# Kernel tuning notes

Hardware: AMD Instinct MI355X
Metric: run time of the kernel (lower is better)

The kernel has to match this reference:

```python
import jax, jax.numpy as jnp
import numpy as np

HIDDEN = 512
HEADS = 8
HEAD_DIM = HIDDEN // HEADS
B, S = 4, 2048
EPS = 1e-5


def setup_inputs() -> dict:
    key = jax.random.key(0)
    ks = jax.random.split(key, 12)
    sc = 1.0 / np.sqrt(HIDDEN)
    return {
        "query": jax.random.normal(ks[0], (B, S, HIDDEN), jnp.float32),
        "key": jax.random.normal(ks[1], (B, S, HIDDEN), jnp.float32),
        "value": jax.random.normal(ks[2], (B, S, HIDDEN), jnp.float32),
        "mask": jnp.ones((B, S), jnp.int32),
        "Wq": jax.random.normal(ks[3], (HIDDEN, HIDDEN), jnp.float32) * sc,
        "bq": jnp.zeros((HIDDEN,), jnp.float32),
        "Wk": jax.random.normal(ks[4], (HIDDEN, HIDDEN), jnp.float32) * sc,
        "bk": jnp.zeros((HIDDEN,), jnp.float32),
        "Wv": jax.random.normal(ks[5], (HIDDEN, HIDDEN), jnp.float32) * sc,
        "bv": jnp.zeros((HIDDEN,), jnp.float32),
        "Wo": jax.random.normal(ks[6], (HIDDEN, HIDDEN), jnp.float32) * sc,
        "bo": jnp.zeros((HIDDEN,), jnp.float32),
        "temperature": jnp.ones((HEADS,), jnp.float32),
        "gamma": jnp.ones((HIDDEN,), jnp.float32),
        "beta": jnp.zeros((HIDDEN,), jnp.float32),
    }


def _split_heads(x):  # (B,S,H*D) -> (B,H,S,D)
    b, s, _ = x.shape
    return x.reshape(b, s, HEADS, HEAD_DIM).transpose(0, 2, 1, 3)


def _l1_scores(Q, K):
    # Manhattan distance dist[b,h,i,j] = sum_d |Q[b,h,i,d] - K[b,h,j,d]|
    # accumulated via scan over head_dim to avoid a (B,H,S,S,D) tensor.
    Qd = jnp.moveaxis(Q, -1, 0)  # (D,B,H,S)
    Kd = jnp.moveaxis(K, -1, 0)
    init = jnp.zeros(Q.shape[:3] + (K.shape[2],), Q.dtype)  # (B,H,S,S)

    def step(acc, qk):
        q, k = qk  # (B,H,S)
        return acc + jnp.abs(q[..., :, None] - k[..., None, :]), None

    dist, _ = jax.lax.scan(step, init, (Qd, Kd))
    return dist


def reference(query, key, value, mask, Wq, bq, Wk, bk, Wv, bv, Wo, bo,
              temperature, gamma, beta):
    Q = _split_heads(query @ Wq.T + bq)
    K = _split_heads(key @ Wk.T + bk)
    V = _split_heads(value @ Wv.T + bv)

    dist = _l1_scores(Q, K)                                 # (B,H,S,S)
    scores = -dist * temperature[None, :, None, None]
    m = mask[:, None, None, :]                              # (B,1,1,S)
    scores = jnp.where(m == 0, jnp.float32(-1e9), scores)
    attn = jax.nn.softmax(scores, axis=-1)                  # (B,H,S,S)

    out = jnp.einsum("bhij,bhjd->bhid", attn, V)            # (B,H,S,D)
    out = out.transpose(0, 2, 1, 3).reshape(query.shape)    # (B,S,HIDDEN)
    out = out @ Wo.T + bo

    res = out + query
    mu = jnp.mean(res, axis=-1, keepdims=True)
    var = jnp.var(res, axis=-1, keepdims=True)
    out = (res - mu) * jax.lax.rsqrt(var + EPS) * gamma + beta
    return out, attn
```

## Files before the change

### kernel.cpp

```cpp
#include <hip/hip_runtime.h>
#include <math.h>

#define BB 4
#define SS 2048
#define NH 8
#define HD 64
#define HID 512
#define EPSV 1e-5f

#define NROWS (BB * SS)
#define QKV_ELEMS (BB * NH * SS * HD)
#define TOTROWS (BB * NH * SS)
#define NJT 16

typedef __attribute__((ext_vector_type(8))) short short8;
typedef __attribute__((ext_vector_type(4))) float f32x4;

__device__ __forceinline__ unsigned short f2h(float f) {
  _Float16 h = (_Float16)f;
  return __builtin_bit_cast(unsigned short, h);
}
__device__ __forceinline__ float h2f(unsigned short u) {
  return (float)__builtin_bit_cast(_Float16, u);
}

__device__ __forceinline__ void sad2(unsigned qa, unsigned kb, unsigned& acc) {
  asm("v_sad_u16 %0, %1, %2, %0" : "+v"(acc) : "v"(qa), "v"(kb));
}

__device__ __forceinline__ unsigned pk_mul_f16(unsigned a, unsigned b) {
  unsigned r;
  asm("v_pk_mul_f16 %0, %1, %2" : "=v"(r) : "v"(a), "v"(b));
  return r;
}

__global__ __launch_bounds__(256, 2) void qkv_proj_kernel(
    const float* __restrict__ query, const float* __restrict__ key,
    const float* __restrict__ value, const float* __restrict__ Wq,
    const float* __restrict__ Wk, const float* __restrict__ Wv,
    const float* __restrict__ bq, const float* __restrict__ bk,
    const float* __restrict__ bv, unsigned short* __restrict__ Qh,
    unsigned short* __restrict__ Kh, unsigned short* __restrict__ Vt) {
  __shared__ unsigned short As[128][40];
  __shared__ unsigned short Ws[128][40];
  const int z = blockIdx.z;
  const float* A = (z == 0) ? query : (z == 1) ? key : value;
  const float* W = (z == 0) ? Wq : (z == 1) ? Wk : Wv;
  const float* bias = (z == 0) ? bq : (z == 1) ? bk : bv;
  unsigned short* Cout = (z == 0) ? Qh : (z == 1) ? Kh : Vt;

  const int m0 = blockIdx.y * 128;
  const int n0 = blockIdx.x * 128;
  const int tid = threadIdx.x;
  const int lane = tid & 63;
  const int w = tid >> 6;
  const int wr = w >> 1;
  const int wc = w & 1;
  const int l16 = lane & 15;
  const int lq = lane >> 4;

  f32x4 acc[4][4];
#pragma unroll
  for (int mr = 0; mr < 4; ++mr)
#pragma unroll
    for (int nc = 0; nc < 4; ++nc) acc[mr][nc] = (f32x4)0.f;

  for (int k0 = 0; k0 < HID; k0 += 32) {
    __syncthreads();
#pragma unroll
    for (int p = 0; p < 4; ++p) {
      int idx = tid + p * 256;
      int row = idx >> 3;
      int c4 = (idx & 7) * 4;
      float4 av = *(const float4*)&A[(size_t)(m0 + row) * HID + k0 + c4];
      float4 wv = *(const float4*)&W[(size_t)(n0 + row) * HID + k0 + c4];
      ushort4 ab = {f2h(av.x), f2h(av.y), f2h(av.z), f2h(av.w)};
      ushort4 wb = {f2h(wv.x), f2h(wv.y), f2h(wv.z), f2h(wv.w)};
      *(ushort4*)&As[row][c4] = ab;
      *(ushort4*)&Ws[row][c4] = wb;
    }
    __syncthreads();
    const int kb = lq * 8;
    short8 a[4], b[4];
#pragma unroll
    for (int mr = 0; mr < 4; ++mr)
      a[mr] = *(const short8*)&As[wr * 64 + mr * 16 + l16][kb];
#pragma unroll
    for (int nc = 0; nc < 4; ++nc)
      b[nc] = *(const short8*)&Ws[wc * 64 + nc * 16 + l16][kb];
#pragma unroll
    for (int mr = 0; mr < 4; ++mr)
#pragma unroll
      for (int nc = 0; nc < 4; ++nc)
        acc[mr][nc] = __builtin_amdgcn_mfma_f32_16x16x32_f16(a[mr], b[nc], acc[mr][nc], 0, 0, 0);
  }

#pragma unroll
  for (int nc = 0; nc < 4; ++nc) {
    const int n = n0 + wc * 64 + nc * 16 + l16;
    const float bv_ = bias[n];
#pragma unroll
    for (int mr = 0; mr < 4; ++mr) {
#pragma unroll
      for (int jj = 0; jj < 4; ++jj) {
        const int m = m0 + wr * 64 + mr * 16 + lq * 4 + jj;
        float v = acc[mr][nc][jj] + bv_;
        const int b_ = m >> 11, s = m & (SS - 1);
        const int h = n >> 6, d = n & 63;
        if (z == 2) {
          Cout[(((size_t)(b_ * NH + h)) * HD + d) * SS + s] = f2h(v);
        } else {
          int u = (int)floorf(fmaf(v, 4096.f, 32768.5f));
          u = u < 0 ? 0 : (u > 65535 ? 65535 : u);
          Cout[(((size_t)(b_ * NH + h)) * SS + s) * HD + d] = (unsigned short)u;
        }
      }
    }
  }
}

__global__ __launch_bounds__(256, 2) void gemm_out(const unsigned short* __restrict__ A,
                                                   const float* __restrict__ W,
                                                   const float* __restrict__ bias,
                                                   float* __restrict__ Cout) {
  __shared__ unsigned short As[128][40];
  __shared__ unsigned short Ws[128][40];
  const int m0 = blockIdx.y * 128;
  const int n0 = blockIdx.x * 128;
  const int tid = threadIdx.x;
  const int lane = tid & 63;
  const int w = tid >> 6;
  const int wr = w >> 1;
  const int wc = w & 1;
  const int l16 = lane & 15;
  const int lq = lane >> 4;

  f32x4 acc[4][4];
#pragma unroll
  for (int mr = 0; mr < 4; ++mr)
#pragma unroll
    for (int nc = 0; nc < 4; ++nc) acc[mr][nc] = (f32x4)0.f;

  for (int k0 = 0; k0 < HID; k0 += 32) {
    __syncthreads();
#pragma unroll
    for (int p = 0; p < 2; ++p) {
      int idx = tid + p * 256;
      int row = idx >> 2;
      int ch = (idx & 3) * 8;
      *(uint4*)&As[row][ch] = *(const uint4*)&A[(size_t)(m0 + row) * HID + k0 + ch];
    }
#pragma unroll
    for (int p = 0; p < 4; ++p) {
      int idx = tid + p * 256;
      int row = idx >> 3;
      int c4 = (idx & 7) * 4;
      float4 wv = *(const float4*)&W[(size_t)(n0 + row) * HID + k0 + c4];
      ushort4 wb = {f2h(wv.x), f2h(wv.y), f2h(wv.z), f2h(wv.w)};
      *(ushort4*)&Ws[row][c4] = wb;
    }
    __syncthreads();
    const int kb = lq * 8;
    short8 a[4], b[4];
#pragma unroll
    for (int mr = 0; mr < 4; ++mr)
      a[mr] = *(const short8*)&As[wr * 64 + mr * 16 + l16][kb];
#pragma unroll
    for (int nc = 0; nc < 4; ++nc)
      b[nc] = *(const short8*)&Ws[wc * 64 + nc * 16 + l16][kb];
#pragma unroll
    for (int mr = 0; mr < 4; ++mr)
#pragma unroll
      for (int nc = 0; nc < 4; ++nc)
        acc[mr][nc] = __builtin_amdgcn_mfma_f32_16x16x32_f16(a[mr], b[nc], acc[mr][nc], 0, 0, 0);
  }

#pragma unroll
  for (int nc = 0; nc < 4; ++nc) {
    const int n = n0 + wc * 64 + nc * 16 + l16;
    const float bv = bias[n];
#pragma unroll
    for (int mr = 0; mr < 4; ++mr)
#pragma unroll
      for (int jj = 0; jj < 4; ++jj) {
        const int m = m0 + wr * 64 + mr * 16 + lq * 4 + jj;
        Cout[(size_t)m * HID + n] = acc[mr][nc][jj] + bv;
      }
  }
}

__global__ __launch_bounds__(512, 4) void scores_kernel(
    const unsigned short* __restrict__ Qh, const unsigned short* __restrict__ Kh,
    const int* __restrict__ mask, const float* __restrict__ temp,
    float* __restrict__ attn, float* __restrict__ stats,
    float* __restrict__ msnap) {
  __shared__ unsigned short Ks[128][72];
  __shared__ int Ms[128];

  const int bh = blockIdx.y;
  const int b = bh >> 3;
  const int h = bh & 7;
  const int i0 = blockIdx.x * 128;
  const int tid = threadIdx.x;
  const int trow = tid >> 4;
  const int cg = tid & 15;
  const float tscale = temp[h] * (1.0f / 4096.0f);

  const unsigned short* Qb = Qh + (size_t)bh * SS * HD;
  const unsigned short* Kb = Kh + (size_t)bh * SS * HD;
  float* attn_b = attn + (size_t)bh * SS * SS;

  float m[4], sg[4];
#pragma unroll
  for (int rr = 0; rr < 4; ++rr) {
    m[rr] = -INFINITY;
    sg[rr] = 0.f;
  }

  for (int j0 = 0; j0 < SS; j0 += 128) {
    __syncthreads();
#pragma unroll
    for (int p = 0; p < 2; ++p) {
      int idx = tid + p * 512;
      int row = idx >> 3;
      int ch = (idx & 7) * 8;
      *(uint4*)&Ks[row][ch] = *(const uint4*)&Kb[(size_t)(j0 + row) * HD + ch];
    }
    if (tid < 128) Ms[tid] = mask[b * SS + j0 + tid];
    __syncthreads();

    unsigned d[4][8];
#pragma unroll
    for (int rr = 0; rr < 4; ++rr)
#pragma unroll
      for (int c = 0; c < 8; ++c) d[rr][c] = 0u;

#pragma unroll 2
    for (int k8 = 0; k8 < 8; ++k8) {
      uint4 q4[4];
#pragma unroll
      for (int rr = 0; rr < 4; ++rr)
        q4[rr] = *(const uint4*)&Qb[(size_t)(i0 + trow + 32 * rr) * HD + k8 * 8];
#pragma unroll
      for (int c = 0; c < 8; ++c) {
        const uint4 kx = *(const uint4*)&Ks[cg + 16 * c][k8 * 8];
#pragma unroll
        for (int rr = 0; rr < 4; ++rr) {
          sad2(q4[rr].x, kx.x, d[rr][c]);
          sad2(q4[rr].y, kx.y, d[rr][c]);
          sad2(q4[rr].z, kx.z, d[rr][c]);
          sad2(q4[rr].w, kx.w, d[rr][c]);
        }
      }
    }

    int msk[8];
#pragma unroll
    for (int c = 0; c < 8; ++c) msk[c] = Ms[cg + 16 * c];

    const int jt = j0 >> 7;
#pragma unroll
    for (int rr = 0; rr < 4; ++rr) {
      float s[8];
      float rmax = -INFINITY;
#pragma unroll
      for (int c = 0; c < 8; ++c) {
        float sc = -(float)d[rr][c] * tscale;
        if (msk[c] == 0) sc = -1e9f;
        s[c] = sc;
        rmax = fmaxf(rmax, sc);
      }
#pragma unroll
      for (int off = 1; off < 16; off <<= 1) rmax = fmaxf(rmax, __shfl_xor(rmax, off));
      const float mnew = fmaxf(m[rr], rmax);
      const int i = i0 + trow + 32 * rr;
      unsigned short* arow = (unsigned short*)(attn_b + (size_t)i * SS);
      float psum = 0.f;
#pragma unroll
      for (int c = 0; c < 8; ++c) {
        float pv = __expf(s[c] - mnew);
        psum += pv;
        arow[2048 + j0 + cg + 16 * c] = f2h(pv);
      }
      sg[rr] = sg[rr] * __expf(m[rr] - mnew) + psum;
      m[rr] = mnew;
      if (cg == 0) msnap[((size_t)bh * NJT + jt) * SS + i] = mnew;
    }
  }

#pragma unroll
  for (int rr = 0; rr < 4; ++rr) {
    float ssum = sg[rr];
#pragma unroll
    for (int off = 1; off < 16; off <<= 1) ssum += __shfl_xor(ssum, off);
    if (cg == 0) {
      const int row = bh * SS + i0 + trow + 32 * rr;
      stats[2 * row] = m[rr];
      stats[2 * row + 1] = ssum;
    }
  }
}

__global__ __launch_bounds__(512, 2) void attn_pv_norm_kernel(
    const unsigned short* __restrict__ Vt, const float* __restrict__ stats,
    const float* __restrict__ msnap, float* __restrict__ attn,
    unsigned short* __restrict__ attn_out) {
  __shared__ unsigned short Ps[128][72];
  __shared__ unsigned short Vts[64][72];
  __shared__ float corr_s[128];

  const int bh = blockIdx.y;
  const int b = bh >> 3;
  const int h = bh & 7;
  const int i0 = blockIdx.x * 128;
  const int tid = threadIdx.x;
  const int lane = tid & 63;
  const int w = tid >> 6;
  const int wr = w >> 1;
  const int wc = w & 1;
  const int l16 = lane & 15;
  const int lq = lane >> 4;

  float* attn_b = attn + (size_t)bh * SS * SS;
  const unsigned short* Vtb = Vt + (size_t)bh * HD * SS;

  float mfin = 0.f, inv = 0.f;
  if (tid < 128) {
    const int row = bh * SS + i0 + tid;
    mfin = stats[2 * row];
    inv = 1.0f / stats[2 * row + 1];
  }

  f32x4 acc[2][2];
#pragma unroll
  for (int mr = 0; mr < 2; ++mr)
#pragma unroll
    for (int nc = 0; nc < 2; ++nc) acc[mr][nc] = (f32x4)0.f;

  for (int j0 = 0; j0 < SS; j0 += 64) {
    __syncthreads();
    if (tid < 128)
      corr_s[tid] =
          __expf(msnap[((size_t)bh * NJT + (j0 >> 7)) * SS + i0 + tid] - mfin) * inv;
    {
      int row = tid >> 3;
      int ch = (tid & 7) * 8;
      *(uint4*)&Vts[row][ch] = *(const uint4*)&Vtb[(size_t)row * SS + j0 + ch];
    }
    uint4 pv[2];
#pragma unroll
    for (int p = 0; p < 2; ++p) {
      int idx = tid + p * 512;
      int row = idx >> 3;
      int ch = (idx & 7) * 8;
      pv[p] = *(const uint4*)((const unsigned short*)(attn_b + (size_t)(i0 + row) * SS) +
                              2048 + j0 + ch);
    }
    __syncthreads();
#pragma unroll
    for (int p = 0; p < 2; ++p) {
      int idx = tid + p * 512;
      int row = idx >> 3;
      int ch = (idx & 7) * 8;
      const float cr = corr_s[row];
      unsigned short cu = f2h(cr);
      unsigned c2 = (unsigned)cu | ((unsigned)cu << 16);
      uint4 r;
      r.x = pk_mul_f16(pv[p].x, c2);
      r.y = pk_mul_f16(pv[p].y, c2);
      r.z = pk_mul_f16(pv[p].z, c2);
      r.w = pk_mul_f16(pv[p].w, c2);
      *(uint4*)&Ps[row][ch] = r;
      float* orow = attn_b + (size_t)(i0 + row) * SS + j0 + ch;
      float4 o0 = {h2f((unsigned short)(pv[p].x)) * cr,
                   h2f((unsigned short)(pv[p].x >> 16)) * cr,
                   h2f((unsigned short)(pv[p].y)) * cr,
                   h2f((unsigned short)(pv[p].y >> 16)) * cr};
      float4 o1 = {h2f((unsigned short)(pv[p].z)) * cr,
                   h2f((unsigned short)(pv[p].z >> 16)) * cr,
                   h2f((unsigned short)(pv[p].w)) * cr,
                   h2f((unsigned short)(pv[p].w >> 16)) * cr};
      *(float4*)&orow[0] = o0;
      *(float4*)&orow[4] = o1;
    }
    __syncthreads();
#pragma unroll
    for (int ks = 0; ks < 2; ++ks) {
      const int kb = ks * 32 + lq * 8;
      short8 a[2], bf[2];
#pragma unroll
      for (int mr = 0; mr < 2; ++mr)
        a[mr] = *(const short8*)&Ps[wr * 32 + mr * 16 + l16][kb];
#pragma unroll
      for (int nc = 0; nc < 2; ++nc)
        bf[nc] = *(const short8*)&Vts[wc * 32 + nc * 16 + l16][kb];
#pragma unroll
      for (int mr = 0; mr < 2; ++mr)
#pragma unroll
        for (int nc = 0; nc < 2; ++nc)
          acc[mr][nc] = __builtin_amdgcn_mfma_f32_16x16x32_f16(a[mr], bf[nc], acc[mr][nc], 0, 0, 0);
    }
  }

#pragma unroll
  for (int mr = 0; mr < 2; ++mr)
#pragma unroll
    for (int nc = 0; nc < 2; ++nc)
#pragma unroll
      for (int jj = 0; jj < 4; ++jj) {
        const int i = i0 + wr * 32 + mr * 16 + lq * 4 + jj;
        const int d = wc * 32 + nc * 16 + l16;
        attn_out[((size_t)(b * SS + i)) * HID + h * HD + d] = f2h(acc[mr][nc][jj]);
      }
}

__global__ __launch_bounds__(256) void ln_kernel(const float* __restrict__ proj,
                                                 const float* __restrict__ query,
                                                 const float* __restrict__ gamma,
                                                 const float* __restrict__ beta,
                                                 float* __restrict__ out) {
  const int row = blockIdx.x;
  const int tid = threadIdx.x;

  float x[2];
  float sum = 0.f, sumsq = 0.f;
#pragma unroll
  for (int t = 0; t < 2; ++t) {
    const int c = tid + t * 256;
    float v = proj[(size_t)row * HID + c] + query[(size_t)row * HID + c];
    x[t] = v;
    sum += v;
    sumsq += v * v;
  }
#pragma unroll
  for (int off = 1; off < 64; off <<= 1) {
    sum += __shfl_xor(sum, off);
    sumsq += __shfl_xor(sumsq, off);
  }
  __shared__ float s1[4], s2[4];
  if ((tid & 63) == 0) {
    s1[tid >> 6] = sum;
    s2[tid >> 6] = sumsq;
  }
  __syncthreads();
  sum = s1[0] + s1[1] + s1[2] + s1[3];
  sumsq = s2[0] + s2[1] + s2[2] + s2[3];
  const float mu = sum * (1.f / HID);
  const float var = sumsq * (1.f / HID) - mu * mu;
  const float rstd = rsqrtf(var + EPSV);
#pragma unroll
  for (int t = 0; t < 2; ++t) {
    const int c = tid + t * 256;
    out[(size_t)row * HID + c] = (x[t] - mu) * rstd * gamma[c] + beta[c];
  }
}

extern "C" void kernel_launch(void* const* d_in, const int* in_sizes, int n_in,
                              void* d_out, int out_size, void* d_ws, size_t ws_size,
                              hipStream_t stream) {
  const float* query = (const float*)d_in[0];
  const float* key = (const float*)d_in[1];
  const float* value = (const float*)d_in[2];
  const int* mask = (const int*)d_in[3];
  const float* Wq = (const float*)d_in[4];
  const float* bq = (const float*)d_in[5];
  const float* Wk = (const float*)d_in[6];
  const float* bk = (const float*)d_in[7];
  const float* Wv = (const float*)d_in[8];
  const float* bv = (const float*)d_in[9];
  const float* Wo = (const float*)d_in[10];
  const float* bo = (const float*)d_in[11];
  const float* temp = (const float*)d_in[12];
  const float* gamma = (const float*)d_in[13];
  const float* beta = (const float*)d_in[14];

  float* out_final = (float*)d_out;
  float* attn = (float*)d_out + (size_t)BB * SS * HID;

  unsigned short* Qh = (unsigned short*)d_ws;
  unsigned short* Kh = Qh + QKV_ELEMS;
  unsigned short* Vt = Kh + QKV_ELEMS;
  unsigned short* aout = Vt + QKV_ELEMS;
  float* stats = (float*)(aout + QKV_ELEMS);
  float* msnap = stats + 2 * TOTROWS;
  float* proj = (float*)d_ws;

  const dim3 blk(256);

  qkv_proj_kernel<<<dim3(HID / 128, NROWS / 128, 3), blk, 0, stream>>>(
      query, key, value, Wq, Wk, Wv, bq, bk, bv, Qh, Kh, Vt);

  const dim3 sgrid(SS / 128, BB * NH);
  scores_kernel<<<sgrid, dim3(512), 0, stream>>>(Qh, Kh, mask, temp, attn, stats, msnap);

  const dim3 pgrid(SS / 128, BB * NH);
  attn_pv_norm_kernel<<<pgrid, dim3(512), 0, stream>>>(Vt, stats, msnap, attn, aout);

  gemm_out<<<dim3(HID / 128, NROWS / 128), blk, 0, stream>>>(aout, Wo, bo, proj);
  ln_kernel<<<NROWS, blk, 0, stream>>>(proj, query, gamma, beta, out_final);
}
```

Measured before the change: 556.9 us.

## Fuse L1 scores and PV/normalize kernels into one attention kernel

Merges the scores kernel and the PV/normalization kernel into a single kernel per 128-row tile, so each row block does both phases back to back. Per-tile running maxima and final max/sum stats stay in shared memory instead of going through global msnap/stats buffers, and the K tile buffer is reused for the scaled probabilities. This removes one launch and the global stats traffic, and the fp16 probabilities may still be cached when read back. The cost is a serial dependency inside each block and a launch bound of 4 blocks per CU carried over from the scores kernel, which may pressure registers in the MFMA phase.

```diff
diff --git a/kernel.cpp b/kernel.cpp
--- a/kernel.cpp
+++ b/kernel.cpp
@@ -189,12 +189,17 @@
   }
 }
 
-__global__ __launch_bounds__(512, 4) void scores_kernel(
+__global__ __launch_bounds__(512, 4) void attn_fused_kernel(
     const unsigned short* __restrict__ Qh, const unsigned short* __restrict__ Kh,
-    const int* __restrict__ mask, const float* __restrict__ temp,
-    float* __restrict__ attn, float* __restrict__ stats,
-    float* __restrict__ msnap) {
-  __shared__ unsigned short Ks[128][72];
+    const unsigned short* __restrict__ Vt, const int* __restrict__ mask,
+    const float* __restrict__ temp, float* __restrict__ attn,
+    unsigned short* __restrict__ attn_out) {
+  __shared__ unsigned short KP[128][72];
+  __shared__ unsigned short Vts[64][72];
+  __shared__ float msnap_s[NJT][128];
+  __shared__ float mfin_s[128];
+  __shared__ float inv_s[128];
+  __shared__ float corr_s[128];
   __shared__ int Ms[128];
 
   const int bh = blockIdx.y;
@@ -202,216 +207,201 @@
   const int h = bh & 7;
   const int i0 = blockIdx.x * 128;
   const int tid = threadIdx.x;
-  const int trow = tid >> 4;
-  const int cg = tid & 15;
   const float tscale = temp[h] * (1.0f / 4096.0f);
 
   const unsigned short* Qb = Qh + (size_t)bh * SS * HD;
   const unsigned short* Kb = Kh + (size_t)bh * SS * HD;
+  const unsigned short* Vtb = Vt + (size_t)bh * HD * SS;
   float* attn_b = attn + (size_t)bh * SS * SS;
 
-  float m[4], sg[4];
-#pragma unroll
-  for (int rr = 0; rr < 4; ++rr) {
-    m[rr] = -INFINITY;
-    sg[rr] = 0.f;
-  }
-
-  for (int j0 = 0; j0 < SS; j0 += 128) {
-    __syncthreads();
-#pragma unroll
-    for (int p = 0; p < 2; ++p) {
-      int idx = tid + p * 512;
-      int row = idx >> 3;
-      int ch = (idx & 7) * 8;
-      *(uint4*)&Ks[row][ch] = *(const uint4*)&Kb[(size_t)(j0 + row) * HD + ch];
-    }
-    if (tid < 128) Ms[tid] = mask[b * SS + j0 + tid];
-    __syncthreads();
-
-    unsigned d[4][8];
-#pragma unroll
-    for (int rr = 0; rr < 4; ++rr)
-#pragma unroll
-      for (int c = 0; c < 8; ++c) d[rr][c] = 0u;
+  {
+    const int trow = tid >> 4;
+    const int cg = tid & 15;
+
+    float m[4], sg[4];
+#pragma unroll
+    for (int rr = 0; rr < 4; ++rr) {
+      m[rr] = -INFINITY;
+      sg[rr] = 0.f;
+    }
+
+    for (int j0 = 0; j0 < SS; j0 += 128) {
+      __syncthreads();
+#pragma unroll
+      for (int p = 0; p < 2; ++p) {
+        int idx = tid + p * 512;
+        int row = idx >> 3;
+        int ch = (idx & 7) * 8;
+        *(uint4*)&KP[row][ch] = *(const uint4*)&Kb[(size_t)(j0 + row) * HD + ch];
+      }
+      if (tid < 128) Ms[tid] = mask[b * SS + j0 + tid];
+      __syncthreads();
+
+      unsigned d[4][8];
+#pragma unroll
+      for (int rr = 0; rr < 4; ++rr)
+#pragma unroll
+        for (int c = 0; c < 8; ++c) d[rr][c] = 0u;
 
 #pragma unroll 2
-    for (int k8 = 0; k8 < 8; ++k8) {
-      uint4 q4[4];
-#pragma unroll
-      for (int rr = 0; rr < 4; ++rr)
-        q4[rr] = *(const uint4*)&Qb[(size_t)(i0 + trow + 32 * rr) * HD + k8 * 8];
-#pragma unroll
-      for (int c = 0; c < 8; ++c) {
-        const uint4 kx = *(const uint4*)&Ks[cg + 16 * c][k8 * 8];
-#pragma unroll
-        for (int rr = 0; rr < 4; ++rr) {
-          sad2(q4[rr].x, kx.x, d[rr][c]);
-          sad2(q4[rr].y, kx.y, d[rr][c]);
-          sad2(q4[rr].z, kx.z, d[rr][c]);
-          sad2(q4[rr].w, kx.w, d[rr][c]);
+      for (int k8 = 0; k8 < 8; ++k8) {
+        uint4 q4[4];
+#pragma unroll
+        for (int rr = 0; rr < 4; ++rr)
+          q4[rr] = *(const uint4*)&Qb[(size_t)(i0 + trow + 32 * rr) * HD + k8 * 8];
+#pragma unroll
+        for (int c = 0; c < 8; ++c) {
+          const uint4 kx = *(const uint4*)&KP[cg + 16 * c][k8 * 8];
+#pragma unroll
+          for (int rr = 0; rr < 4; ++rr) {
+            sad2(q4[rr].x, kx.x, d[rr][c]);
+            sad2(q4[rr].y, kx.y, d[rr][c]);
+            sad2(q4[rr].z, kx.z, d[rr][c]);
+            sad2(q4[rr].w, kx.w, d[rr][c]);
+          }
         }
       }
-    }
-
-    int msk[8];
-#pragma unroll
-    for (int c = 0; c < 8; ++c) msk[c] = Ms[cg + 16 * c];
-
-    const int jt = j0 >> 7;
+
+      int msk[8];
+#pragma unroll
+      for (int c = 0; c < 8; ++c) msk[c] = Ms[cg + 16 * c];
+
+      const int jt = j0 >> 7;
+#pragma unroll
+      for (int rr = 0; rr < 4; ++rr) {
+        float s[8];
+        float rmax = -INFINITY;
+#pragma unroll
+        for (int c = 0; c < 8; ++c) {
+          float sc = -(float)d[rr][c] * tscale;
+          if (msk[c] == 0) sc = -1e9f;
+          s[c] = sc;
+          rmax = fmaxf(rmax, sc);
+        }
+#pragma unroll
+        for (int off = 1; off < 16; off <<= 1)
+          rmax = fmaxf(rmax, __shfl_xor(rmax, off));
+        const float mnew = fmaxf(m[rr], rmax);
+        const int i = i0 + trow + 32 * rr;
+        unsigned short* arow = (unsigned short*)(attn_b + (size_t)i * SS);
+        float psum = 0.f;
+#pragma unroll
+        for (int c = 0; c < 8; ++c) {
+          float pv = __expf(s[c] - mnew);
+          psum += pv;
+          arow[2048 + j0 + cg + 16 * c] = f2h(pv);
+        }
+        sg[rr] = sg[rr] * __expf(m[rr] - mnew) + psum;
+        m[rr] = mnew;
+        if (cg == 0) msnap_s[jt][trow + 32 * rr] = mnew;
+      }
+    }
+
 #pragma unroll
     for (int rr = 0; rr < 4; ++rr) {
-      float s[8];
-      float rmax = -INFINITY;
-#pragma unroll
-      for (int c = 0; c < 8; ++c) {
-        float sc = -(float)d[rr][c] * tscale;
-        if (msk[c] == 0) sc = -1e9f;
-        s[c] = sc;
-        rmax = fmaxf(rmax, sc);
-      }
-#pragma unroll
-      for (int off = 1; off < 16; off <<= 1) rmax = fmaxf(rmax, __shfl_xor(rmax, off));
-      const float mnew = fmaxf(m[rr], rmax);
-      const int i = i0 + trow + 32 * rr;
-      unsigned short* arow = (unsigned short*)(attn_b + (size_t)i * SS);
-      float psum = 0.f;
-#pragma unroll
-      for (int c = 0; c < 8; ++c) {
-        float pv = __expf(s[c] - mnew);
-        psum += pv;
-        arow[2048 + j0 + cg + 16 * c] = f2h(pv);
-      }
-      sg[rr] = sg[rr] * __expf(m[rr] - mnew) + psum;
-      m[rr] = mnew;
-      if (cg == 0) msnap[((size_t)bh * NJT + jt) * SS + i] = mnew;
-    }
-  }
-
-#pragma unroll
-  for (int rr = 0; rr < 4; ++rr) {
-    float ssum = sg[rr];
-#pragma unroll
-    for (int off = 1; off < 16; off <<= 1) ssum += __shfl_xor(ssum, off);
-    if (cg == 0) {
-      const int row = bh * SS + i0 + trow + 32 * rr;
-      stats[2 * row] = m[rr];
-      stats[2 * row + 1] = ssum;
-    }
-  }
-}
-
-__global__ __launch_bounds__(512, 2) void attn_pv_norm_kernel(
-    const unsigned short* __restrict__ Vt, const float* __restrict__ stats,
-    const float* __restrict__ msnap, float* __restrict__ attn,
-    unsigned short* __restrict__ attn_out) {
-  __shared__ unsigned short Ps[128][72];
-  __shared__ unsigned short Vts[64][72];
-  __shared__ float corr_s[128];
-
-  const int bh = blockIdx.y;
-  const int b = bh >> 3;
-  const int h = bh & 7;
-  const int i0 = blockIdx.x * 128;
-  const int tid = threadIdx.x;
-  const int lane = tid & 63;
-  const int w = tid >> 6;
-  const int wr = w >> 1;
-  const int wc = w & 1;
-  const int l16 = lane & 15;
-  const int lq = lane >> 4;
-
-  float* attn_b = attn + (size_t)bh * SS * SS;
-  const unsigned short* Vtb = Vt + (size_t)bh * HD * SS;
-
-  float mfin = 0.f, inv = 0.f;
-  if (tid < 128) {
-    const int row = bh * SS + i0 + tid;
-    mfin = stats[2 * row];
-    inv = 1.0f / stats[2 * row + 1];
-  }
-
-  f32x4 acc[2][2];
-#pragma unroll
-  for (int mr = 0; mr < 2; ++mr)
-#pragma unroll
-    for (int nc = 0; nc < 2; ++nc) acc[mr][nc] = (f32x4)0.f;
-
-  for (int j0 = 0; j0 < SS; j0 += 64) {
-    __syncthreads();
-    if (tid < 128)
-      corr_s[tid] =
-          __expf(msnap[((size_t)bh * NJT + (j0 >> 7)) * SS + i0 + tid] - mfin) * inv;
-    {
-      int row = tid >> 3;
-      int ch = (tid & 7) * 8;
-      *(uint4*)&Vts[row][ch] = *(const uint4*)&Vtb[(size_t)row * SS + j0 + ch];
-    }
-    uint4 pv[2];
-#pragma unroll
-    for (int p = 0; p < 2; ++p) {
-      int idx = tid + p * 512;
-      int row = idx >> 3;
-      int ch = (idx & 7) * 8;
-      pv[p] = *(const uint4*)((const unsigned short*)(attn_b + (size_t)(i0 + row) * SS) +
-                              2048 + j0 + ch);
-    }
-    __syncthreads();
-#pragma unroll
-    for (int p = 0; p < 2; ++p) {
-      int idx = tid + p * 512;
-      int row = idx >> 3;
-      int ch = (idx & 7) * 8;
-      const float cr = corr_s[row];
-      unsigned short cu = f2h(cr);
-      unsigned c2 = (unsigned)cu | ((unsigned)cu << 16);
-      uint4 r;
-      r.x = pk_mul_f16(pv[p].x, c2);
-      r.y = pk_mul_f16(pv[p].y, c2);
-      r.z = pk_mul_f16(pv[p].z, c2);
-      r.w = pk_mul_f16(pv[p].w, c2);
-      *(uint4*)&Ps[row][ch] = r;
-      float* orow = attn_b + (size_t)(i0 + row) * SS + j0 + ch;
-      float4 o0 = {h2f((unsigned short)(pv[p].x)) * cr,
-                   h2f((unsigned short)(pv[p].x >> 16)) * cr,
-                   h2f((unsigned short)(pv[p].y)) * cr,
-                   h2f((unsigned short)(pv[p].y >> 16)) * cr};
-      float4 o1 = {h2f((unsigned short)(pv[p].z)) * cr,
-                   h2f((unsigned short)(pv[p].z >> 16)) * cr,
-                   h2f((unsigned short)(pv[p].w)) * cr,
-                   h2f((unsigned short)(pv[p].w >> 16)) * cr};
-      *(float4*)&orow[0] = o0;
-      *(float4*)&orow[4] = o1;
-    }
-    __syncthreads();
-#pragma unroll
-    for (int ks = 0; ks < 2; ++ks) {
-      const int kb = ks * 32 + lq * 8;
-      short8 a[2], bf[2];
-#pragma unroll
-      for (int mr = 0; mr < 2; ++mr)
-        a[mr] = *(const short8*)&Ps[wr * 32 + mr * 16 + l16][kb];
+      float ssum = sg[rr];
+#pragma unroll
+      for (int off = 1; off < 16; off <<= 1) ssum += __shfl_xor(ssum, off);
+      if (cg == 0) {
+        mfin_s[trow + 32 * rr] = m[rr];
+        inv_s[trow + 32 * rr] = 1.0f / ssum;
+      }
+    }
+  }
+
+  __syncthreads();
+
+  {
+    const int lane = tid & 63;
+    const int w = tid >> 6;
+    const int wr = w >> 1;
+    const int wc = w & 1;
+    const int l16 = lane & 15;
+    const int lq = lane >> 4;
+
+    f32x4 acc[2][2];
+#pragma unroll
+    for (int mr = 0; mr < 2; ++mr)
+#pragma unroll
+      for (int nc = 0; nc < 2; ++nc) acc[mr][nc] = (f32x4)0.f;
+
+    for (int j0 = 0; j0 < SS; j0 += 64) {
+      __syncthreads();
+      if (tid < 128)
+        corr_s[tid] = __expf(msnap_s[j0 >> 7][tid] - mfin_s[tid]) * inv_s[tid];
+      {
+        int row = tid >> 3;
+        int ch = (tid & 7) * 8;
+        *(uint4*)&Vts[row][ch] = *(const uint4*)&Vtb[(size_t)row * SS + j0 + ch];
+      }
+      uint4 pv[2];
+#pragma unroll
+      for (int p = 0; p < 2; ++p) {
+        int idx = tid + p * 512;
+        int row = idx >> 3;
+        int ch = (idx & 7) * 8;
+        pv[p] = *(const uint4*)((const unsigned short*)(attn_b +
+                                                        (size_t)(i0 + row) * SS) +
+                                2048 + j0 + ch);
+      }
+      __syncthreads();
+#pragma unroll
+      for (int p = 0; p < 2; ++p) {
+        int idx = tid + p * 512;
+        int row = idx >> 3;
+        int ch = (idx & 7) * 8;
+        const float cr = corr_s[row];
+        unsigned short cu = f2h(cr);
+        unsigned c2 = (unsigned)cu | ((unsigned)cu << 16);
+        uint4 r;
+        r.x = pk_mul_f16(pv[p].x, c2);
+        r.y = pk_mul_f16(pv[p].y, c2);
+        r.z = pk_mul_f16(pv[p].z, c2);
+        r.w = pk_mul_f16(pv[p].w, c2);
+        *(uint4*)&KP[row][ch] = r;
+        float* orow = attn_b + (size_t)(i0 + row) * SS + j0 + ch;
+        float4 o0 = {h2f((unsigned short)(pv[p].x)) * cr,
+                     h2f((unsigned short)(pv[p].x >> 16)) * cr,
+                     h2f((unsigned short)(pv[p].y)) * cr,
+                     h2f((unsigned short)(pv[p].y >> 16)) * cr};
+        float4 o1 = {h2f((unsigned short)(pv[p].z)) * cr,
+                     h2f((unsigned short)(pv[p].z >> 16)) * cr,
+                     h2f((unsigned short)(pv[p].w)) * cr,
+                     h2f((unsigned short)(pv[p].w >> 16)) * cr};
+        *(float4*)&orow[0] = o0;
+        *(float4*)&orow[4] = o1;
+      }
+      __syncthreads();
+#pragma unroll
+      for (int ks = 0; ks < 2; ++ks) {
+        const int kb = ks * 32 + lq * 8;
+        short8 a[2], bf[2];
+#pragma unroll
+        for (int mr = 0; mr < 2; ++mr)
+          a[mr] = *(const short8*)&KP[wr * 32 + mr * 16 + l16][kb];
+#pragma unroll
+        for (int nc = 0; nc < 2; ++nc)
+          bf[nc] = *(const short8*)&Vts[wc * 32 + nc * 16 + l16][kb];
+#pragma unroll
+        for (int mr = 0; mr < 2; ++mr)
+#pragma unroll
+          for (int nc = 0; nc < 2; ++nc)
+            acc[mr][nc] =
+                __builtin_amdgcn_mfma_f32_16x16x32_f16(a[mr], bf[nc], acc[mr][nc], 0, 0, 0);
+      }
+    }
+
+#pragma unroll
+    for (int mr = 0; mr < 2; ++mr)
 #pragma unroll
       for (int nc = 0; nc < 2; ++nc)
-        bf[nc] = *(const short8*)&Vts[wc * 32 + nc * 16 + l16][kb];
-#pragma unroll
-      for (int mr = 0; mr < 2; ++mr)
-#pragma unroll
-        for (int nc = 0; nc < 2; ++nc)
-          acc[mr][nc] = __builtin_amdgcn_mfma_f32_16x16x32_f16(a[mr], bf[nc], acc[mr][nc], 0, 0, 0);
-    }
-  }
-
-#pragma unroll
-  for (int mr = 0; mr < 2; ++mr)
-#pragma unroll
-    for (int nc = 0; nc < 2; ++nc)
-#pragma unroll
-      for (int jj = 0; jj < 4; ++jj) {
-        const int i = i0 + wr * 32 + mr * 16 + lq * 4 + jj;
-        const int d = wc * 32 + nc * 16 + l16;
-        attn_out[((size_t)(b * SS + i)) * HID + h * HD + d] = f2h(acc[mr][nc][jj]);
-      }
+#pragma unroll
+        for (int jj = 0; jj < 4; ++jj) {
+          const int i = i0 + wr * 32 + mr * 16 + lq * 4 + jj;
+          const int d = wc * 32 + nc * 16 + l16;
+          attn_out[((size_t)(b * SS + i)) * HID + h * HD + d] = f2h(acc[mr][nc][jj]);
+        }
+  }
 }
 
 __global__ __launch_bounds__(256) void ln_kernel(const float* __restrict__ proj,
@@ -481,8 +471,6 @@
   unsigned short* Kh = Qh + QKV_ELEMS;
   unsigned short* Vt = Kh + QKV_ELEMS;
   unsigned short* aout = Vt + QKV_ELEMS;
-  float* stats = (float*)(aout + QKV_ELEMS);
-  float* msnap = stats + 2 * TOTROWS;
   float* proj = (float*)d_ws;
 
   const dim3 blk(256);
@@ -490,11 +478,8 @@
   qkv_proj_kernel<<<dim3(HID / 128, NROWS / 128, 3), blk, 0, stream>>>(
       query, key, value, Wq, Wk, Wv, bq, bk, bv, Qh, Kh, Vt);
 
-  const dim3 sgrid(SS / 128, BB * NH);
-  scores_kernel<<<sgrid, dim3(512), 0, stream>>>(Qh, Kh, mask, temp, attn, stats, msnap);
-
-  const dim3 pgrid(SS / 128, BB * NH);
-  attn_pv_norm_kernel<<<pgrid, dim3(512), 0, stream>>>(Vt, stats, msnap, attn, aout);
+  attn_fused_kernel<<<dim3(SS / 128, BB * NH), dim3(512), 0, stream>>>(
+      Qh, Kh, Vt, mask, temp, attn, aout);
 
   gemm_out<<<dim3(HID / 128, NROWS / 128), blk, 0, stream>>>(aout, Wo, bo, proj);
   ln_kernel<<<NROWS, blk, 0, stream>>>(proj, query, gamma, beta, out_final);
```

Result: faster. 483.4 us, median of 2 (-13.2%).
